# Optimization experiments

Hardware: AMD Instinct MI355X
Metric: run time of the kernel (lower is better)

## Reference

```python
import jax, jax.numpy as jnp
import numpy as np

BN_EPS = 1e-3  # Keras BatchNormalization default epsilon

def _conv2d_same(x, w, b):
    # x: NHWC, w: HWIO (kh,kw,2,1)
    y = jax.lax.conv_general_dilated(x, w, window_strides=(1, 1), padding='SAME',
                                     dimension_numbers=('NHWC', 'HWIO', 'NHWC'))
    return y + b

def _zpool(t):
    # concat([max, avg], axis=-1) over channel axis -> last dim = 2
    return jnp.concatenate([jnp.max(t, axis=-1, keepdims=True),
                            jnp.mean(t, axis=-1, keepdims=True)], axis=-1)

def _att_map(t2, w, b, g, beta, mean, var):
    y = _conv2d_same(t2, w, b)
    y = (y - mean) * jax.lax.rsqrt(var + BN_EPS) * g + beta  # inference BN
    return jax.nn.sigmoid(y)

def setup_inputs() -> dict:
    key = jax.random.key(0)
    ks = jax.random.split(key, 8)
    B, H, W, C, K, RR = 32, 56, 56, 256, 7, 8
    d = {}
    d['x'] = jax.random.normal(ks[0], (B, H, W, C), dtype=jnp.float32)
    for i, kk in zip((1, 2, 3), ks[1:4]):
        d[f'conv{i}_w'] = jax.random.normal(kk, (K, K, 2, 1), dtype=jnp.float32) * 0.1
        d[f'conv{i}_b'] = jnp.zeros((1,), dtype=jnp.float32)
        d[f'bn{i}_g'] = jnp.ones((1,), dtype=jnp.float32)
        d[f'bn{i}_b'] = jnp.zeros((1,), dtype=jnp.float32)
        d[f'bn{i}_m'] = jnp.zeros((1,), dtype=jnp.float32)
        d[f'bn{i}_v'] = jnp.ones((1,), dtype=jnp.float32)
    Ch = C // RR
    d['se_w1'] = jax.random.normal(ks[4], (C, Ch), dtype=jnp.float32) * (2.0 / C) ** 0.5
    d['se_b1'] = jnp.zeros((Ch,), dtype=jnp.float32)
    d['se_w2'] = jax.random.normal(ks[5], (Ch, C), dtype=jnp.float32) * 0.05
    d['se_b2'] = jnp.zeros((C,), dtype=jnp.float32)
    return d

def reference(x, conv1_w, conv1_b, bn1_g, bn1_b, bn1_m, bn1_v,
              conv2_w, conv2_b, bn2_g, bn2_b, bn2_m, bn2_v,
              conv3_w, conv3_b, bn3_g, bn3_b, bn3_m, bn3_v,
              se_w1, se_b1, se_w2, se_b2):
    # Branch 1 (H-axis): permute (B,H,W,C)->(B,H,C,W), pool over W
    th1 = jnp.transpose(x, (0, 1, 3, 2))
    a1 = _att_map(_zpool(th1), conv1_w, conv1_b, bn1_g, bn1_b, bn1_m, bn1_v)
    br1 = jnp.transpose(th1 * a1, (0, 1, 3, 2))
    # Branch 2 (W-axis): permute (B,H,W,C)->(B,C,W,H), pool over H
    th2 = jnp.transpose(x, (0, 3, 2, 1))
    a2 = _att_map(_zpool(th2), conv2_w, conv2_b, bn2_g, bn2_b, bn2_m, bn2_v)
    br2 = jnp.transpose(th2 * a2, (0, 3, 2, 1))
    # Branch 3 (identity): pool over C
    a3 = _att_map(_zpool(x), conv3_w, conv3_b, bn3_g, bn3_b, bn3_m, bn3_v)
    br3 = x * a3
    # TriSE1: Add branches, then SE channel gating
    s = br1 + br2 + br3
    gap = jnp.mean(s, axis=(1, 2), keepdims=True)            # (B,1,1,C)
    h = jax.nn.relu(jnp.einsum('bijc,cd->bijd', gap, se_w1) + se_b1)
    cw = jax.nn.sigmoid(jnp.einsum('bijd,dc->bijc', h, se_w2) + se_b2)
    return s * cw
```

## Files before the change

kernel.cpp:

```cpp
#include <hip/hip_runtime.h>
#include <math.h>

namespace {
constexpr int B = 32, H = 56, W = 56, C = 256;
constexpr int HW  = H * W;
constexpr int WC  = W * C;
constexpr int HC  = H * C;
constexpr int HWC = H * W * C;
constexpr int CH  = 32;
constexpr float BN_EPS = 1e-3f;

__device__ __forceinline__ float sigmoidf_(float v) { return 1.0f / (1.0f + expf(-v)); }
}

__global__ __launch_bounds__(256)
void pool13_kernel(const float* __restrict__ x,
                   float* __restrict__ pmax1, float* __restrict__ pavg1,
                   float* __restrict__ pmax3, float* __restrict__ pavg3) {
    const int b = blockIdx.x / H, h = blockIdx.x % H;
    const int t = threadIdx.x;
    const int lane = t & 63, sub = t >> 6;
    const int c4 = lane * 4;
    const float* xp = x + (size_t)b * HWC + (size_t)h * WC;

    float4 mx = make_float4(-INFINITY, -INFINITY, -INFINITY, -INFINITY);
    float4 sm = make_float4(0.f, 0.f, 0.f, 0.f);
    for (int wq = 0; wq < 14; ++wq) {
        const int w = wq * 4 + sub;
        const float4 v = *(const float4*)(xp + w * C + c4);
        mx.x = fmaxf(mx.x, v.x); mx.y = fmaxf(mx.y, v.y);
        mx.z = fmaxf(mx.z, v.z); mx.w = fmaxf(mx.w, v.w);
        sm.x += v.x; sm.y += v.y; sm.z += v.z; sm.w += v.w;
        float m3 = fmaxf(fmaxf(v.x, v.y), fmaxf(v.z, v.w));
        float s3 = v.x + v.y + v.z + v.w;
        #pragma unroll
        for (int off = 32; off > 0; off >>= 1) {
            m3 = fmaxf(m3, __shfl_down(m3, off));
            s3 += __shfl_down(s3, off);
        }
        if (lane == 0) {
            pmax3[b * HW + h * W + w] = m3;
            pavg3[b * HW + h * W + w] = s3 * (1.0f / C);
        }
    }
    __shared__ float smx[4][256];
    __shared__ float ssm[4][256];
    *(float4*)&smx[sub][c4] = mx;
    *(float4*)&ssm[sub][c4] = sm;
    __syncthreads();
    const float m = fmaxf(fmaxf(smx[0][t], smx[1][t]), fmaxf(smx[2][t], smx[3][t]));
    const float s = ssm[0][t] + ssm[1][t] + ssm[2][t] + ssm[3][t];
    pmax1[b * HC + h * C + t] = m;
    pavg1[b * HC + h * C + t] = s * (1.0f / W);
}

__global__ __launch_bounds__(256)
void pool2_kernel(const float* __restrict__ x,
                  float* __restrict__ pmax2, float* __restrict__ pavg2) {
    const int b = blockIdx.x / W, w = blockIdx.x % W;
    const int t = threadIdx.x;
    const int lane = t & 63, sub = t >> 6;
    const int c4 = lane * 4;
    const float* xp = x + (size_t)b * HWC + (size_t)w * C;

    float4 mx = make_float4(-INFINITY, -INFINITY, -INFINITY, -INFINITY);
    float4 sm = make_float4(0.f, 0.f, 0.f, 0.f);
    for (int hq = 0; hq < 14; ++hq) {
        const int h = hq * 4 + sub;
        const float4 v = *(const float4*)(xp + (size_t)h * WC + c4);
        mx.x = fmaxf(mx.x, v.x); mx.y = fmaxf(mx.y, v.y);
        mx.z = fmaxf(mx.z, v.z); mx.w = fmaxf(mx.w, v.w);
        sm.x += v.x; sm.y += v.y; sm.z += v.z; sm.w += v.w;
    }
    __shared__ float smx[4][256];
    __shared__ float ssm[4][256];
    *(float4*)&smx[sub][c4] = mx;
    *(float4*)&ssm[sub][c4] = sm;
    __syncthreads();
    const float m = fmaxf(fmaxf(smx[0][t], smx[1][t]), fmaxf(smx[2][t], smx[3][t]));
    const float s = ssm[0][t] + ssm[1][t] + ssm[2][t] + ssm[3][t];
    pmax2[b * WC + w * C + t] = m;
    pavg2[b * WC + w * C + t] = s * (1.0f / H);
}

__global__ __launch_bounds__(256)
void conv1_kernel(const float* __restrict__ pmax, const float* __restrict__ pavg,
                  const float* __restrict__ cwt, const float* __restrict__ cb,
                  const float* __restrict__ g, const float* __restrict__ beta,
                  const float* __restrict__ mean, const float* __restrict__ var,
                  float* __restrict__ a1) {
    const int b = blockIdx.x / H, h = blockIdx.x % H;
    const int c = threadIdx.x;
    __shared__ float wg[98];
    if (c < 98) wg[c] = cwt[c];
    __syncthreads();
    const float A  = rsqrtf(var[0] + BN_EPS) * g[0];
    const float Bc = (cb[0] - mean[0]) * A + beta[0];
    float acc = 0.f;
    const float* bm = pmax + b * HC;
    const float* ba = pavg + b * HC;
    #pragma unroll
    for (int ky = 0; ky < 7; ++ky) {
        const int hy = h + ky - 3;
        if (hy < 0 || hy >= H) continue;
        const float* rm = bm + hy * C;
        const float* ra = ba + hy * C;
        #pragma unroll
        for (int kx = 0; kx < 7; ++kx) {
            const int cx = c + kx - 3;
            if (cx < 0 || cx >= C) continue;
            acc += rm[cx] * wg[ky * 14 + kx * 2] + ra[cx] * wg[ky * 14 + kx * 2 + 1];
        }
    }
    a1[b * HC + h * C + c] = sigmoidf_(acc * A + Bc);
}

__global__ __launch_bounds__(256)
void conv2_kernel(const float* __restrict__ pmax, const float* __restrict__ pavg,
                  const float* __restrict__ cwt, const float* __restrict__ cb,
                  const float* __restrict__ g, const float* __restrict__ beta,
                  const float* __restrict__ mean, const float* __restrict__ var,
                  float* __restrict__ a2t) {
    const int b = blockIdx.x / W, w = blockIdx.x % W;
    const int c = threadIdx.x;
    __shared__ float wg[98];
    if (c < 98) wg[c] = cwt[c];
    __syncthreads();
    const float A  = rsqrtf(var[0] + BN_EPS) * g[0];
    const float Bc = (cb[0] - mean[0]) * A + beta[0];
    float acc = 0.f;
    #pragma unroll
    for (int kx = 0; kx < 7; ++kx) {
        const int wx = w + kx - 3;
        if (wx < 0 || wx >= W) continue;
        const float* rm = pmax + b * WC + wx * C;
        const float* ra = pavg + b * WC + wx * C;
        #pragma unroll
        for (int ky = 0; ky < 7; ++ky) {
            const int cy = c + ky - 3;
            if (cy < 0 || cy >= C) continue;
            acc += rm[cy] * wg[ky * 14 + kx * 2] + ra[cy] * wg[ky * 14 + kx * 2 + 1];
        }
    }
    a2t[b * WC + w * C + c] = sigmoidf_(acc * A + Bc);
}

__global__ __launch_bounds__(256)
void conv3_kernel(const float* __restrict__ pmax, const float* __restrict__ pavg,
                  const float* __restrict__ cwt, const float* __restrict__ cb,
                  const float* __restrict__ g, const float* __restrict__ beta,
                  const float* __restrict__ mean, const float* __restrict__ var,
                  float* __restrict__ a3) {
    const int b = blockIdx.x / 13;
    const int idx = (blockIdx.x % 13) * 256 + threadIdx.x;
    __shared__ float wg[98];
    if (threadIdx.x < 98) wg[threadIdx.x] = cwt[threadIdx.x];
    __syncthreads();
    if (idx >= HW) return;
    const int h = idx / W, w = idx % W;
    const float A  = rsqrtf(var[0] + BN_EPS) * g[0];
    const float Bc = (cb[0] - mean[0]) * A + beta[0];
    float acc = 0.f;
    const float* bm = pmax + b * HW;
    const float* ba = pavg + b * HW;
    #pragma unroll
    for (int ky = 0; ky < 7; ++ky) {
        const int hy = h + ky - 3;
        if (hy < 0 || hy >= H) continue;
        #pragma unroll
        for (int kx = 0; kx < 7; ++kx) {
            const int wx = w + kx - 3;
            if (wx < 0 || wx >= W) continue;
            acc += bm[hy * W + wx] * wg[ky * 14 + kx * 2] + ba[hy * W + wx] * wg[ky * 14 + kx * 2 + 1];
        }
    }
    a3[b * HW + idx] = sigmoidf_(acc * A + Bc);
}

__global__ __launch_bounds__(256)
void gap_kernel(const float* __restrict__ x, const float* __restrict__ a1,
                const float* __restrict__ a2t, const float* __restrict__ a3,
                float* __restrict__ gap) {
    const int b = blockIdx.x / H, h = blockIdx.x % H;
    const int t = threadIdx.x;
    const int lane = t & 63, sub = t >> 6;
    const int c4 = lane * 4;
    const float* xp  = x   + (size_t)b * HWC + (size_t)h * WC;
    const float* a2b = a2t + (size_t)b * WC;
    const float4 a1v = *(const float4*)(a1 + b * HC + h * C + c4);
    float4 acc = make_float4(0.f, 0.f, 0.f, 0.f);
    for (int wq = 0; wq < 14; ++wq) {
        const int w = wq * 4 + sub;
        const float4 xv  = *(const float4*)(xp  + w * C + c4);
        const float4 a2v = *(const float4*)(a2b + w * C + c4);
        const float a3v  = a3[b * HW + h * W + w];
        acc.x += xv.x * (a1v.x + a2v.x + a3v);
        acc.y += xv.y * (a1v.y + a2v.y + a3v);
        acc.z += xv.z * (a1v.z + a2v.z + a3v);
        acc.w += xv.w * (a1v.w + a2v.w + a3v);
    }
    __shared__ float sacc[4][256];
    *(float4*)&sacc[sub][c4] = acc;
    __syncthreads();
    const float s = sacc[0][t] + sacc[1][t] + sacc[2][t] + sacc[3][t];
    atomicAdd(&gap[b * C + t], s * (1.0f / (float)HW));
}

__global__ __launch_bounds__(256)
void se_kernel(const float* __restrict__ gap,
               const float* __restrict__ w1, const float* __restrict__ b1,
               const float* __restrict__ w2, const float* __restrict__ b2,
               float* __restrict__ cw) {
    const int b = blockIdx.x;
    const int t = threadIdx.x;
    __shared__ float gs[C];
    __shared__ float hs[CH];
    gs[t] = gap[b * C + t];
    __syncthreads();
    if (t < CH) {
        float a = b1[t];
        for (int c = 0; c < C; ++c) a += gs[c] * w1[c * CH + t];
        hs[t] = fmaxf(a, 0.f);
    }
    __syncthreads();
    float a = b2[t];
    #pragma unroll
    for (int d = 0; d < CH; ++d) a += hs[d] * w2[d * C + t];
    cw[b * C + t] = sigmoidf_(a);
}

__global__ __launch_bounds__(256)
void out_kernel(const float* __restrict__ x, const float* __restrict__ a1,
                const float* __restrict__ a2t, const float* __restrict__ a3,
                const float* __restrict__ cw, float* __restrict__ out) {
    const int r = blockIdx.x * 4 + (threadIdx.x >> 6);
    const int b = r / HW;
    const int hw = r % HW;
    const int h = hw / W, w = hw % W;
    const int c = (threadIdx.x & 63) * 4;
    const float4 xv  = *(const float4*)(x   + (size_t)r * C + c);
    const float4 a1v = *(const float4*)(a1  + b * HC + h * C + c);
    const float4 a2v = *(const float4*)(a2t + b * WC + w * C + c);
    const float  a3v = a3[r];
    const float4 cwv = *(const float4*)(cw  + b * C + c);
    float4 o;
    o.x = xv.x * (a1v.x + a2v.x + a3v) * cwv.x;
    o.y = xv.y * (a1v.y + a2v.y + a3v) * cwv.y;
    o.z = xv.z * (a1v.z + a2v.z + a3v) * cwv.z;
    o.w = xv.w * (a1v.w + a2v.w + a3v) * cwv.w;
    *(float4*)(out + (size_t)r * C + c) = o;
}

extern "C" void kernel_launch(void* const* d_in, const int* in_sizes, int n_in,
                              void* d_out, int out_size, void* d_ws, size_t ws_size,
                              hipStream_t stream) {
    const float* x = (const float*)d_in[0];
    const float* c1w = (const float*)d_in[1];  const float* c1b = (const float*)d_in[2];
    const float* g1  = (const float*)d_in[3];  const float* be1 = (const float*)d_in[4];
    const float* m1  = (const float*)d_in[5];  const float* v1  = (const float*)d_in[6];
    const float* c2w = (const float*)d_in[7];  const float* c2b = (const float*)d_in[8];
    const float* g2  = (const float*)d_in[9];  const float* be2 = (const float*)d_in[10];
    const float* m2  = (const float*)d_in[11]; const float* v2  = (const float*)d_in[12];
    const float* c3w = (const float*)d_in[13]; const float* c3b = (const float*)d_in[14];
    const float* g3  = (const float*)d_in[15]; const float* be3 = (const float*)d_in[16];
    const float* m3  = (const float*)d_in[17]; const float* v3  = (const float*)d_in[18];
    const float* sw1 = (const float*)d_in[19]; const float* sb1 = (const float*)d_in[20];
    const float* sw2 = (const float*)d_in[21]; const float* sb2 = (const float*)d_in[22];

    float* ws = (float*)d_ws;
    float* pmax1 = ws;
    float* pavg1 = pmax1 + (size_t)B * HC;
    float* pmax2 = pavg1 + (size_t)B * HC;
    float* pavg2 = pmax2 + (size_t)B * WC;
    float* pmax3 = pavg2 + (size_t)B * WC;
    float* pavg3 = pmax3 + (size_t)B * HW;
    float* a1    = pavg3 + (size_t)B * HW;
    float* a2t   = a1    + (size_t)B * HC;
    float* a3    = a2t   + (size_t)B * WC;
    float* gap   = a3    + (size_t)B * HW;
    float* cwv   = gap   + (size_t)B * C;

    hipMemsetAsync(gap, 0, (size_t)B * C * sizeof(float), stream);

    pool13_kernel<<<B * H, 256, 0, stream>>>(x, pmax1, pavg1, pmax3, pavg3);
    pool2_kernel <<<B * W, 256, 0, stream>>>(x, pmax2, pavg2);
    conv1_kernel <<<B * H, 256, 0, stream>>>(pmax1, pavg1, c1w, c1b, g1, be1, m1, v1, a1);
    conv2_kernel <<<B * W, 256, 0, stream>>>(pmax2, pavg2, c2w, c2b, g2, be2, m2, v2, a2t);
    conv3_kernel <<<B * 13, 256, 0, stream>>>(pmax3, pavg3, c3w, c3b, g3, be3, m3, v3, a3);
    gap_kernel   <<<B * H, 256, 0, stream>>>(x, a1, a2t, a3, gap);
    se_kernel    <<<B, 256, 0, stream>>>(gap, sw1, sb1, sw2, sb2, cwv);
    out_kernel   <<<B * HW / 4, 256, 0, stream>>>(x, a1, a2t, a3, cwv, (float*)d_out);
}
```

Before: 325.9 us.

## Fuse all stages into one persistent cooperative kernel with grid syncs

Replaces the eight separate launches and the memset with a single cooperative persistent kernel. Its blocks loop over task lists for pooling, the three convolutions, the GAP partial sums, the SE MLP and the output, with grid.sync between phases. The GAP atomics become per-task partial sums that are reduced deterministically in the SE phase. This is meant to remove launch overhead and tail gaps between small kernels. In exchange it adds grid-wide barriers, limits the grid size to occupancy, and leaves most blocks idle during the SE phase, which only B blocks run.

```diff
diff --git a/kernel.cpp b/kernel.cpp
--- a/kernel.cpp
+++ b/kernel.cpp
@@ -1,5 +1,8 @@
 #include <hip/hip_runtime.h>
+#include <hip/hip_cooperative_groups.h>
 #include <math.h>
+
+namespace cg = cooperative_groups;
 
 namespace {
 constexpr int B = 32, H = 56, W = 56, C = 256;
@@ -10,251 +13,258 @@
 constexpr int CH  = 32;
 constexpr float BN_EPS = 1e-3f;
 
+constexpr int NPOOL_TASKS = 2 * B * H;
+constexpr int NCONV_TASKS = B * H + B * W + (B * HW) / 256;
+constexpr int NHALF_TASKS = B * H * 2;
+
 __device__ __forceinline__ float sigmoidf_(float v) { return 1.0f / (1.0f + expf(-v)); }
 }
 
-__global__ __launch_bounds__(256)
-void pool13_kernel(const float* __restrict__ x,
-                   float* __restrict__ pmax1, float* __restrict__ pavg1,
-                   float* __restrict__ pmax3, float* __restrict__ pavg3) {
-    const int b = blockIdx.x / H, h = blockIdx.x % H;
-    const int t = threadIdx.x;
-    const int lane = t & 63, sub = t >> 6;
-    const int c4 = lane * 4;
-    const float* xp = x + (size_t)b * HWC + (size_t)h * WC;
-
-    float4 mx = make_float4(-INFINITY, -INFINITY, -INFINITY, -INFINITY);
-    float4 sm = make_float4(0.f, 0.f, 0.f, 0.f);
-    for (int wq = 0; wq < 14; ++wq) {
-        const int w = wq * 4 + sub;
-        const float4 v = *(const float4*)(xp + w * C + c4);
-        mx.x = fmaxf(mx.x, v.x); mx.y = fmaxf(mx.y, v.y);
-        mx.z = fmaxf(mx.z, v.z); mx.w = fmaxf(mx.w, v.w);
-        sm.x += v.x; sm.y += v.y; sm.z += v.z; sm.w += v.w;
-        float m3 = fmaxf(fmaxf(v.x, v.y), fmaxf(v.z, v.w));
-        float s3 = v.x + v.y + v.z + v.w;
-        #pragma unroll
-        for (int off = 32; off > 0; off >>= 1) {
-            m3 = fmaxf(m3, __shfl_down(m3, off));
-            s3 += __shfl_down(s3, off);
-        }
-        if (lane == 0) {
-            pmax3[b * HW + h * W + w] = m3;
-            pavg3[b * HW + h * W + w] = s3 * (1.0f / C);
-        }
-    }
+__global__ __launch_bounds__(256, 4)
+void fused_trise_kernel(const float* __restrict__ x,
+                        const float* __restrict__ c1w, const float* __restrict__ c1b,
+                        const float* __restrict__ g1,  const float* __restrict__ be1,
+                        const float* __restrict__ m1,  const float* __restrict__ v1,
+                        const float* __restrict__ c2w, const float* __restrict__ c2b,
+                        const float* __restrict__ g2,  const float* __restrict__ be2,
+                        const float* __restrict__ m2,  const float* __restrict__ v2,
+                        const float* __restrict__ c3w, const float* __restrict__ c3b,
+                        const float* __restrict__ g3,  const float* __restrict__ be3,
+                        const float* __restrict__ m3,  const float* __restrict__ v3,
+                        const float* __restrict__ sw1, const float* __restrict__ sb1,
+                        const float* __restrict__ sw2, const float* __restrict__ sb2,
+                        float* __restrict__ ws, float* __restrict__ out) {
+    float* pmax1 = ws;
+    float* pavg1 = pmax1 + (size_t)B * HC;
+    float* pmax2 = pavg1 + (size_t)B * HC;
+    float* pavg2 = pmax2 + (size_t)B * WC;
+    float* pmax3 = pavg2 + (size_t)B * WC;
+    float* pavg3 = pmax3 + (size_t)B * HW;
+    float* a1    = pavg3 + (size_t)B * HW;
+    float* a2t   = a1    + (size_t)B * HC;
+    float* a3    = a2t   + (size_t)B * WC;
+    float* gpart = a3    + (size_t)B * HW;
+    float* cw    = gpart + (size_t)NHALF_TASKS * C;
+
     __shared__ float smx[4][256];
     __shared__ float ssm[4][256];
-    *(float4*)&smx[sub][c4] = mx;
-    *(float4*)&ssm[sub][c4] = sm;
-    __syncthreads();
-    const float m = fmaxf(fmaxf(smx[0][t], smx[1][t]), fmaxf(smx[2][t], smx[3][t]));
-    const float s = ssm[0][t] + ssm[1][t] + ssm[2][t] + ssm[3][t];
-    pmax1[b * HC + h * C + t] = m;
-    pavg1[b * HC + h * C + t] = s * (1.0f / W);
-}
-
-__global__ __launch_bounds__(256)
-void pool2_kernel(const float* __restrict__ x,
-                  float* __restrict__ pmax2, float* __restrict__ pavg2) {
-    const int b = blockIdx.x / W, w = blockIdx.x % W;
-    const int t = threadIdx.x;
+    __shared__ float wc0[98], wc1[98], wc2[98];
+    __shared__ float sbnA[3], sbnB[3];
+    __shared__ float gs[C];
+    __shared__ float hsh[CH];
+
+    const int nb   = gridDim.x;
+    const int t    = threadIdx.x;
     const int lane = t & 63, sub = t >> 6;
-    const int c4 = lane * 4;
-    const float* xp = x + (size_t)b * HWC + (size_t)w * C;
-
-    float4 mx = make_float4(-INFINITY, -INFINITY, -INFINITY, -INFINITY);
-    float4 sm = make_float4(0.f, 0.f, 0.f, 0.f);
-    for (int hq = 0; hq < 14; ++hq) {
-        const int h = hq * 4 + sub;
-        const float4 v = *(const float4*)(xp + (size_t)h * WC + c4);
-        mx.x = fmaxf(mx.x, v.x); mx.y = fmaxf(mx.y, v.y);
-        mx.z = fmaxf(mx.z, v.z); mx.w = fmaxf(mx.w, v.w);
-        sm.x += v.x; sm.y += v.y; sm.z += v.z; sm.w += v.w;
-    }
-    __shared__ float smx[4][256];
-    __shared__ float ssm[4][256];
-    *(float4*)&smx[sub][c4] = mx;
-    *(float4*)&ssm[sub][c4] = sm;
-    __syncthreads();
-    const float m = fmaxf(fmaxf(smx[0][t], smx[1][t]), fmaxf(smx[2][t], smx[3][t]));
-    const float s = ssm[0][t] + ssm[1][t] + ssm[2][t] + ssm[3][t];
-    pmax2[b * WC + w * C + t] = m;
-    pavg2[b * WC + w * C + t] = s * (1.0f / H);
-}
-
-__global__ __launch_bounds__(256)
-void conv1_kernel(const float* __restrict__ pmax, const float* __restrict__ pavg,
-                  const float* __restrict__ cwt, const float* __restrict__ cb,
-                  const float* __restrict__ g, const float* __restrict__ beta,
-                  const float* __restrict__ mean, const float* __restrict__ var,
-                  float* __restrict__ a1) {
-    const int b = blockIdx.x / H, h = blockIdx.x % H;
-    const int c = threadIdx.x;
-    __shared__ float wg[98];
-    if (c < 98) wg[c] = cwt[c];
-    __syncthreads();
-    const float A  = rsqrtf(var[0] + BN_EPS) * g[0];
-    const float Bc = (cb[0] - mean[0]) * A + beta[0];
-    float acc = 0.f;
-    const float* bm = pmax + b * HC;
-    const float* ba = pavg + b * HC;
-    #pragma unroll
-    for (int ky = 0; ky < 7; ++ky) {
-        const int hy = h + ky - 3;
-        if (hy < 0 || hy >= H) continue;
-        const float* rm = bm + hy * C;
-        const float* ra = ba + hy * C;
+    const int c4   = lane * 4;
+
+    if (t < 98) { wc0[t] = c1w[t]; wc1[t] = c2w[t]; wc2[t] = c3w[t]; }
+    if (t == 0) { float A = rsqrtf(v1[0] + BN_EPS) * g1[0]; sbnA[0] = A; sbnB[0] = (c1b[0] - m1[0]) * A + be1[0]; }
+    if (t == 1) { float A = rsqrtf(v2[0] + BN_EPS) * g2[0]; sbnA[1] = A; sbnB[1] = (c2b[0] - m2[0]) * A + be2[0]; }
+    if (t == 2) { float A = rsqrtf(v3[0] + BN_EPS) * g3[0]; sbnA[2] = A; sbnB[2] = (c3b[0] - m3[0]) * A + be3[0]; }
+
+    cg::grid_group grid = cg::this_grid();
+
+    for (int tt = blockIdx.x; tt < NPOOL_TASKS; tt += nb) {
+        if (tt < B * H) {
+            const int b = tt / H, h = tt % H;
+            const float* xp = x + (size_t)b * HWC + (size_t)h * WC;
+            float4 mx = make_float4(-INFINITY, -INFINITY, -INFINITY, -INFINITY);
+            float4 sm = make_float4(0.f, 0.f, 0.f, 0.f);
+            for (int wq = 0; wq < 14; ++wq) {
+                const int w = wq * 4 + sub;
+                const float4 v = *(const float4*)(xp + w * C + c4);
+                mx.x = fmaxf(mx.x, v.x); mx.y = fmaxf(mx.y, v.y);
+                mx.z = fmaxf(mx.z, v.z); mx.w = fmaxf(mx.w, v.w);
+                sm.x += v.x; sm.y += v.y; sm.z += v.z; sm.w += v.w;
+                float m3v = fmaxf(fmaxf(v.x, v.y), fmaxf(v.z, v.w));
+                float s3v = v.x + v.y + v.z + v.w;
+                #pragma unroll
+                for (int off = 32; off > 0; off >>= 1) {
+                    m3v = fmaxf(m3v, __shfl_down(m3v, off));
+                    s3v += __shfl_down(s3v, off);
+                }
+                if (lane == 0) {
+                    pmax3[b * HW + h * W + w] = m3v;
+                    pavg3[b * HW + h * W + w] = s3v * (1.0f / C);
+                }
+            }
+            __syncthreads();
+            *(float4*)&smx[sub][c4] = mx;
+            *(float4*)&ssm[sub][c4] = sm;
+            __syncthreads();
+            const float m = fmaxf(fmaxf(smx[0][t], smx[1][t]), fmaxf(smx[2][t], smx[3][t]));
+            const float s = ssm[0][t] + ssm[1][t] + ssm[2][t] + ssm[3][t];
+            pmax1[b * HC + h * C + t] = m;
+            pavg1[b * HC + h * C + t] = s * (1.0f / W);
+        } else {
+            const int tt2 = tt - B * H;
+            const int b = tt2 / W, w = tt2 % W;
+            const float* xp = x + (size_t)b * HWC + (size_t)w * C;
+            float4 mx = make_float4(-INFINITY, -INFINITY, -INFINITY, -INFINITY);
+            float4 sm = make_float4(0.f, 0.f, 0.f, 0.f);
+            for (int hq = 0; hq < 14; ++hq) {
+                const int h = hq * 4 + sub;
+                const float4 v = *(const float4*)(xp + (size_t)h * WC + c4);
+                mx.x = fmaxf(mx.x, v.x); mx.y = fmaxf(mx.y, v.y);
+                mx.z = fmaxf(mx.z, v.z); mx.w = fmaxf(mx.w, v.w);
+                sm.x += v.x; sm.y += v.y; sm.z += v.z; sm.w += v.w;
+            }
+            __syncthreads();
+            *(float4*)&smx[sub][c4] = mx;
+            *(float4*)&ssm[sub][c4] = sm;
+            __syncthreads();
+            const float m = fmaxf(fmaxf(smx[0][t], smx[1][t]), fmaxf(smx[2][t], smx[3][t]));
+            const float s = ssm[0][t] + ssm[1][t] + ssm[2][t] + ssm[3][t];
+            pmax2[b * WC + w * C + t] = m;
+            pavg2[b * WC + w * C + t] = s * (1.0f / H);
+        }
+    }
+    __threadfence();
+    grid.sync();
+
+    for (int tt = blockIdx.x; tt < NCONV_TASKS; tt += nb) {
+        if (tt < B * H) {
+            const int b = tt / H, h = tt % H;
+            const int c = t;
+            const float A = sbnA[0], Bc = sbnB[0];
+            float acc = 0.f;
+            const float* bm = pmax1 + b * HC;
+            const float* ba = pavg1 + b * HC;
+            #pragma unroll
+            for (int ky = 0; ky < 7; ++ky) {
+                const int hy = h + ky - 3;
+                if (hy < 0 || hy >= H) continue;
+                const float* rm = bm + hy * C;
+                const float* ra = ba + hy * C;
+                #pragma unroll
+                for (int kx = 0; kx < 7; ++kx) {
+                    const int cx = c + kx - 3;
+                    if (cx < 0 || cx >= C) continue;
+                    acc += rm[cx] * wc0[ky * 14 + kx * 2] + ra[cx] * wc0[ky * 14 + kx * 2 + 1];
+                }
+            }
+            a1[b * HC + h * C + c] = sigmoidf_(acc * A + Bc);
+        } else if (tt < 2 * B * H) {
+            const int tt2 = tt - B * H;
+            const int b = tt2 / W, w = tt2 % W;
+            const int c = t;
+            const float A = sbnA[1], Bc = sbnB[1];
+            float acc = 0.f;
+            #pragma unroll
+            for (int kx = 0; kx < 7; ++kx) {
+                const int wx = w + kx - 3;
+                if (wx < 0 || wx >= W) continue;
+                const float* rm = pmax2 + b * WC + wx * C;
+                const float* ra = pavg2 + b * WC + wx * C;
+                #pragma unroll
+                for (int ky = 0; ky < 7; ++ky) {
+                    const int cy = c + ky - 3;
+                    if (cy < 0 || cy >= C) continue;
+                    acc += rm[cy] * wc1[ky * 14 + kx * 2] + ra[cy] * wc1[ky * 14 + kx * 2 + 1];
+                }
+            }
+            a2t[b * WC + w * C + c] = sigmoidf_(acc * A + Bc);
+        } else {
+            const int gid = (tt - 2 * B * H) * 256 + t;
+            const int b = gid / HW;
+            const int hw = gid % HW;
+            const int h = hw / W, w = hw % W;
+            const float A = sbnA[2], Bc = sbnB[2];
+            float acc = 0.f;
+            const float* bm = pmax3 + b * HW;
+            const float* ba = pavg3 + b * HW;
+            #pragma unroll
+            for (int ky = 0; ky < 7; ++ky) {
+                const int hy = h + ky - 3;
+                if (hy < 0 || hy >= H) continue;
+                #pragma unroll
+                for (int kx = 0; kx < 7; ++kx) {
+                    const int wx = w + kx - 3;
+                    if (wx < 0 || wx >= W) continue;
+                    acc += bm[hy * W + wx] * wc2[ky * 14 + kx * 2] + ba[hy * W + wx] * wc2[ky * 14 + kx * 2 + 1];
+                }
+            }
+            a3[b * HW + hw] = sigmoidf_(acc * A + Bc);
+        }
+    }
+    __threadfence();
+    grid.sync();
+
+    for (int tt = blockIdx.x; tt < NHALF_TASKS; tt += nb) {
+        const int b = tt / (2 * H);
+        const int rem = tt % (2 * H);
+        const int h = rem >> 1, half = rem & 1;
+        const float* xp  = x   + (size_t)b * HWC + (size_t)h * WC;
+        const float* a2b = a2t + (size_t)b * WC;
+        const float4 a1v = *(const float4*)(a1 + b * HC + h * C + c4);
+        float4 acc = make_float4(0.f, 0.f, 0.f, 0.f);
+        for (int wq = 0; wq < 7; ++wq) {
+            const int w = half * 28 + wq * 4 + sub;
+            const float4 xv  = *(const float4*)(xp  + w * C + c4);
+            const float4 a2v = *(const float4*)(a2b + w * C + c4);
+            const float a3v  = a3[b * HW + h * W + w];
+            acc.x += xv.x * (a1v.x + a2v.x + a3v);
+            acc.y += xv.y * (a1v.y + a2v.y + a3v);
+            acc.z += xv.z * (a1v.z + a2v.z + a3v);
+            acc.w += xv.w * (a1v.w + a2v.w + a3v);
+        }
+        __syncthreads();
+        *(float4*)&smx[sub][c4] = acc;
+        __syncthreads();
+        gpart[(size_t)tt * C + t] = smx[0][t] + smx[1][t] + smx[2][t] + smx[3][t];
+    }
+    __threadfence();
+    grid.sync();
+
+    if (blockIdx.x < B) {
+        const int b = blockIdx.x;
+        float s = 0.f;
+        for (int r = 0; r < 2 * H; ++r) s += gpart[(size_t)(b * 2 * H + r) * C + t];
+        gs[t] = s * (1.0f / (float)HW);
+        __syncthreads();
+        if (t < CH) {
+            float a = sb1[t];
+            for (int c = 0; c < C; ++c) a += gs[c] * sw1[c * CH + t];
+            hsh[t] = fmaxf(a, 0.f);
+        }
+        __syncthreads();
+        float a = sb2[t];
         #pragma unroll
-        for (int kx = 0; kx < 7; ++kx) {
-            const int cx = c + kx - 3;
-            if (cx < 0 || cx >= C) continue;
-            acc += rm[cx] * wg[ky * 14 + kx * 2] + ra[cx] * wg[ky * 14 + kx * 2 + 1];
-        }
-    }
-    a1[b * HC + h * C + c] = sigmoidf_(acc * A + Bc);
-}
-
-__global__ __launch_bounds__(256)
-void conv2_kernel(const float* __restrict__ pmax, const float* __restrict__ pavg,
-                  const float* __restrict__ cwt, const float* __restrict__ cb,
-                  const float* __restrict__ g, const float* __restrict__ beta,
-                  const float* __restrict__ mean, const float* __restrict__ var,
-                  float* __restrict__ a2t) {
-    const int b = blockIdx.x / W, w = blockIdx.x % W;
-    const int c = threadIdx.x;
-    __shared__ float wg[98];
-    if (c < 98) wg[c] = cwt[c];
-    __syncthreads();
-    const float A  = rsqrtf(var[0] + BN_EPS) * g[0];
-    const float Bc = (cb[0] - mean[0]) * A + beta[0];
-    float acc = 0.f;
-    #pragma unroll
-    for (int kx = 0; kx < 7; ++kx) {
-        const int wx = w + kx - 3;
-        if (wx < 0 || wx >= W) continue;
-        const float* rm = pmax + b * WC + wx * C;
-        const float* ra = pavg + b * WC + wx * C;
-        #pragma unroll
-        for (int ky = 0; ky < 7; ++ky) {
-            const int cy = c + ky - 3;
-            if (cy < 0 || cy >= C) continue;
-            acc += rm[cy] * wg[ky * 14 + kx * 2] + ra[cy] * wg[ky * 14 + kx * 2 + 1];
-        }
-    }
-    a2t[b * WC + w * C + c] = sigmoidf_(acc * A + Bc);
-}
-
-__global__ __launch_bounds__(256)
-void conv3_kernel(const float* __restrict__ pmax, const float* __restrict__ pavg,
-                  const float* __restrict__ cwt, const float* __restrict__ cb,
-                  const float* __restrict__ g, const float* __restrict__ beta,
-                  const float* __restrict__ mean, const float* __restrict__ var,
-                  float* __restrict__ a3) {
-    const int b = blockIdx.x / 13;
-    const int idx = (blockIdx.x % 13) * 256 + threadIdx.x;
-    __shared__ float wg[98];
-    if (threadIdx.x < 98) wg[threadIdx.x] = cwt[threadIdx.x];
-    __syncthreads();
-    if (idx >= HW) return;
-    const int h = idx / W, w = idx % W;
-    const float A  = rsqrtf(var[0] + BN_EPS) * g[0];
-    const float Bc = (cb[0] - mean[0]) * A + beta[0];
-    float acc = 0.f;
-    const float* bm = pmax + b * HW;
-    const float* ba = pavg + b * HW;
-    #pragma unroll
-    for (int ky = 0; ky < 7; ++ky) {
-        const int hy = h + ky - 3;
-        if (hy < 0 || hy >= H) continue;
-        #pragma unroll
-        for (int kx = 0; kx < 7; ++kx) {
-            const int wx = w + kx - 3;
-            if (wx < 0 || wx >= W) continue;
-            acc += bm[hy * W + wx] * wg[ky * 14 + kx * 2] + ba[hy * W + wx] * wg[ky * 14 + kx * 2 + 1];
-        }
-    }
-    a3[b * HW + idx] = sigmoidf_(acc * A + Bc);
-}
-
-__global__ __launch_bounds__(256)
-void gap_kernel(const float* __restrict__ x, const float* __restrict__ a1,
-                const float* __restrict__ a2t, const float* __restrict__ a3,
-                float* __restrict__ gap) {
-    const int b = blockIdx.x / H, h = blockIdx.x % H;
-    const int t = threadIdx.x;
-    const int lane = t & 63, sub = t >> 6;
-    const int c4 = lane * 4;
-    const float* xp  = x   + (size_t)b * HWC + (size_t)h * WC;
-    const float* a2b = a2t + (size_t)b * WC;
-    const float4 a1v = *(const float4*)(a1 + b * HC + h * C + c4);
-    float4 acc = make_float4(0.f, 0.f, 0.f, 0.f);
-    for (int wq = 0; wq < 14; ++wq) {
-        const int w = wq * 4 + sub;
-        const float4 xv  = *(const float4*)(xp  + w * C + c4);
-        const float4 a2v = *(const float4*)(a2b + w * C + c4);
-        const float a3v  = a3[b * HW + h * W + w];
-        acc.x += xv.x * (a1v.x + a2v.x + a3v);
-        acc.y += xv.y * (a1v.y + a2v.y + a3v);
-        acc.z += xv.z * (a1v.z + a2v.z + a3v);
-        acc.w += xv.w * (a1v.w + a2v.w + a3v);
-    }
-    __shared__ float sacc[4][256];
-    *(float4*)&sacc[sub][c4] = acc;
-    __syncthreads();
-    const float s = sacc[0][t] + sacc[1][t] + sacc[2][t] + sacc[3][t];
-    atomicAdd(&gap[b * C + t], s * (1.0f / (float)HW));
-}
-
-__global__ __launch_bounds__(256)
-void se_kernel(const float* __restrict__ gap,
-               const float* __restrict__ w1, const float* __restrict__ b1,
-               const float* __restrict__ w2, const float* __restrict__ b2,
-               float* __restrict__ cw) {
-    const int b = blockIdx.x;
-    const int t = threadIdx.x;
-    __shared__ float gs[C];
-    __shared__ float hs[CH];
-    gs[t] = gap[b * C + t];
-    __syncthreads();
-    if (t < CH) {
-        float a = b1[t];
-        for (int c = 0; c < C; ++c) a += gs[c] * w1[c * CH + t];
-        hs[t] = fmaxf(a, 0.f);
-    }
-    __syncthreads();
-    float a = b2[t];
-    #pragma unroll
-    for (int d = 0; d < CH; ++d) a += hs[d] * w2[d * C + t];
-    cw[b * C + t] = sigmoidf_(a);
-}
-
-__global__ __launch_bounds__(256)
-void out_kernel(const float* __restrict__ x, const float* __restrict__ a1,
-                const float* __restrict__ a2t, const float* __restrict__ a3,
-                const float* __restrict__ cw, float* __restrict__ out) {
-    const int r = blockIdx.x * 4 + (threadIdx.x >> 6);
-    const int b = r / HW;
-    const int hw = r % HW;
-    const int h = hw / W, w = hw % W;
-    const int c = (threadIdx.x & 63) * 4;
-    const float4 xv  = *(const float4*)(x   + (size_t)r * C + c);
-    const float4 a1v = *(const float4*)(a1  + b * HC + h * C + c);
-    const float4 a2v = *(const float4*)(a2t + b * WC + w * C + c);
-    const float  a3v = a3[r];
-    const float4 cwv = *(const float4*)(cw  + b * C + c);
-    float4 o;
-    o.x = xv.x * (a1v.x + a2v.x + a3v) * cwv.x;
-    o.y = xv.y * (a1v.y + a2v.y + a3v) * cwv.y;
-    o.z = xv.z * (a1v.z + a2v.z + a3v) * cwv.z;
-    o.w = xv.w * (a1v.w + a2v.w + a3v) * cwv.w;
-    *(float4*)(out + (size_t)r * C + c) = o;
+        for (int d = 0; d < CH; ++d) a += hsh[d] * sw2[d * C + t];
+        cw[b * C + t] = sigmoidf_(a);
+    }
+    __threadfence();
+    grid.sync();
+
+    for (int tt = blockIdx.x; tt < NHALF_TASKS; tt += nb) {
+        const int b = tt / (2 * H);
+        const int rem = tt % (2 * H);
+        const int h = rem >> 1, half = rem & 1;
+        const float* xp  = x   + (size_t)b * HWC + (size_t)h * WC;
+        const float* a2b = a2t + (size_t)b * WC;
+        float*       op  = out + (size_t)b * HWC + (size_t)h * WC;
+        const float4 a1v = *(const float4*)(a1 + b * HC + h * C + c4);
+        const float4 cwv = *(const float4*)(cw + b * C + c4);
+        for (int wq = 0; wq < 7; ++wq) {
+            const int w = half * 28 + wq * 4 + sub;
+            const float4 xv  = *(const float4*)(xp  + w * C + c4);
+            const float4 a2v = *(const float4*)(a2b + w * C + c4);
+            const float a3v  = a3[b * HW + h * W + w];
+            float4 o;
+            o.x = xv.x * (a1v.x + a2v.x + a3v) * cwv.x;
+            o.y = xv.y * (a1v.y + a2v.y + a3v) * cwv.y;
+            o.z = xv.z * (a1v.z + a2v.z + a3v) * cwv.z;
+            o.w = xv.w * (a1v.w + a2v.w + a3v) * cwv.w;
+            *(float4*)(op + w * C + c4) = o;
+        }
+    }
 }
 
 extern "C" void kernel_launch(void* const* d_in, const int* in_sizes, int n_in,
                               void* d_out, int out_size, void* d_ws, size_t ws_size,
                               hipStream_t stream) {
-    const float* x = (const float*)d_in[0];
+    const float* x   = (const float*)d_in[0];
     const float* c1w = (const float*)d_in[1];  const float* c1b = (const float*)d_in[2];
     const float* g1  = (const float*)d_in[3];  const float* be1 = (const float*)d_in[4];
     const float* m1  = (const float*)d_in[5];  const float* v1  = (const float*)d_in[6];
@@ -266,28 +276,23 @@
     const float* m3  = (const float*)d_in[17]; const float* v3  = (const float*)d_in[18];
     const float* sw1 = (const float*)d_in[19]; const float* sb1 = (const float*)d_in[20];
     const float* sw2 = (const float*)d_in[21]; const float* sb2 = (const float*)d_in[22];
-
-    float* ws = (float*)d_ws;
-    float* pmax1 = ws;
-    float* pavg1 = pmax1 + (size_t)B * HC;
-    float* pmax2 = pavg1 + (size_t)B * HC;
-    float* pavg2 = pmax2 + (size_t)B * WC;
-    float* pmax3 = pavg2 + (size_t)B * WC;
-    float* pavg3 = pmax3 + (size_t)B * HW;
-    float* a1    = pavg3 + (size_t)B * HW;
-    float* a2t   = a1    + (size_t)B * HC;
-    float* a3    = a2t   + (size_t)B * WC;
-    float* gap   = a3    + (size_t)B * HW;
-    float* cwv   = gap   + (size_t)B * C;
-
-    hipMemsetAsync(gap, 0, (size_t)B * C * sizeof(float), stream);
-
-    pool13_kernel<<<B * H, 256, 0, stream>>>(x, pmax1, pavg1, pmax3, pavg3);
-    pool2_kernel <<<B * W, 256, 0, stream>>>(x, pmax2, pavg2);
-    conv1_kernel <<<B * H, 256, 0, stream>>>(pmax1, pavg1, c1w, c1b, g1, be1, m1, v1, a1);
-    conv2_kernel <<<B * W, 256, 0, stream>>>(pmax2, pavg2, c2w, c2b, g2, be2, m2, v2, a2t);
-    conv3_kernel <<<B * 13, 256, 0, stream>>>(pmax3, pavg3, c3w, c3b, g3, be3, m3, v3, a3);
-    gap_kernel   <<<B * H, 256, 0, stream>>>(x, a1, a2t, a3, gap);
-    se_kernel    <<<B, 256, 0, stream>>>(gap, sw1, sb1, sw2, sb2, cwv);
-    out_kernel   <<<B * HW / 4, 256, 0, stream>>>(x, a1, a2t, a3, cwv, (float*)d_out);
+    float* ws  = (float*)d_ws;
+    float* out = (float*)d_out;
+
+    int nbpc = 0;
+    hipOccupancyMaxActiveBlocksPerMultiprocessor(&nbpc, fused_trise_kernel, 256, 0);
+    if (nbpc < 1) nbpc = 1;
+    int grid = nbpc * 256;
+    if (grid > NPOOL_TASKS) grid = NPOOL_TASKS;
+
+    void* args[] = {
+        (void*)&x,
+        (void*)&c1w, (void*)&c1b, (void*)&g1, (void*)&be1, (void*)&m1, (void*)&v1,
+        (void*)&c2w, (void*)&c2b, (void*)&g2, (void*)&be2, (void*)&m2, (void*)&v2,
+        (void*)&c3w, (void*)&c3b, (void*)&g3, (void*)&be3, (void*)&m3, (void*)&v3,
+        (void*)&sw1, (void*)&sb1, (void*)&sw2, (void*)&sb2,
+        (void*)&ws, (void*)&out,
+    };
+    hipLaunchCooperativeKernel((const void*)fused_trise_kernel, dim3(grid), dim3(256),
+                               args, 0, stream);
 }
```

Result: slower. 879.1 us (+169.8%).

## Merge pool and conv launches, replace atomic GAP with partials, row-wise output

Applied to the files above, without the earlier changes.

Combines the two pooling kernels into one launch and the three conv kernels into one branch-dispatched launch, cutting the launch count and letting small grids overlap. The global-average-pool atomics and their memset are replaced by per-row partial sums that the SE kernel reduces. The output kernel now processes one row per block, reusing the a1 and cw loads across 14 width steps. The trade-offs are a larger partial-sum workspace and divergent block roles inside the merged kernels.

```diff
diff --git a/kernel.cpp b/kernel.cpp
--- a/kernel.cpp
+++ b/kernel.cpp
@@ -14,173 +14,162 @@
 }
 
 __global__ __launch_bounds__(256)
-void pool13_kernel(const float* __restrict__ x,
-                   float* __restrict__ pmax1, float* __restrict__ pavg1,
-                   float* __restrict__ pmax3, float* __restrict__ pavg3) {
-    const int b = blockIdx.x / H, h = blockIdx.x % H;
+void pool_all_kernel(const float* __restrict__ x,
+                     float* __restrict__ pmax1, float* __restrict__ pavg1,
+                     float* __restrict__ pmax2, float* __restrict__ pavg2,
+                     float* __restrict__ pmax3, float* __restrict__ pavg3) {
     const int t = threadIdx.x;
     const int lane = t & 63, sub = t >> 6;
     const int c4 = lane * 4;
-    const float* xp = x + (size_t)b * HWC + (size_t)h * WC;
-
-    float4 mx = make_float4(-INFINITY, -INFINITY, -INFINITY, -INFINITY);
-    float4 sm = make_float4(0.f, 0.f, 0.f, 0.f);
-    for (int wq = 0; wq < 14; ++wq) {
-        const int w = wq * 4 + sub;
-        const float4 v = *(const float4*)(xp + w * C + c4);
-        mx.x = fmaxf(mx.x, v.x); mx.y = fmaxf(mx.y, v.y);
-        mx.z = fmaxf(mx.z, v.z); mx.w = fmaxf(mx.w, v.w);
-        sm.x += v.x; sm.y += v.y; sm.z += v.z; sm.w += v.w;
-        float m3 = fmaxf(fmaxf(v.x, v.y), fmaxf(v.z, v.w));
-        float s3 = v.x + v.y + v.z + v.w;
-        #pragma unroll
-        for (int off = 32; off > 0; off >>= 1) {
-            m3 = fmaxf(m3, __shfl_down(m3, off));
-            s3 += __shfl_down(s3, off);
-        }
-        if (lane == 0) {
-            pmax3[b * HW + h * W + w] = m3;
-            pavg3[b * HW + h * W + w] = s3 * (1.0f / C);
-        }
-    }
     __shared__ float smx[4][256];
     __shared__ float ssm[4][256];
-    *(float4*)&smx[sub][c4] = mx;
-    *(float4*)&ssm[sub][c4] = sm;
-    __syncthreads();
-    const float m = fmaxf(fmaxf(smx[0][t], smx[1][t]), fmaxf(smx[2][t], smx[3][t]));
-    const float s = ssm[0][t] + ssm[1][t] + ssm[2][t] + ssm[3][t];
-    pmax1[b * HC + h * C + t] = m;
-    pavg1[b * HC + h * C + t] = s * (1.0f / W);
-}
-
-__global__ __launch_bounds__(256)
-void pool2_kernel(const float* __restrict__ x,
-                  float* __restrict__ pmax2, float* __restrict__ pavg2) {
-    const int b = blockIdx.x / W, w = blockIdx.x % W;
-    const int t = threadIdx.x;
-    const int lane = t & 63, sub = t >> 6;
-    const int c4 = lane * 4;
-    const float* xp = x + (size_t)b * HWC + (size_t)w * C;
-
-    float4 mx = make_float4(-INFINITY, -INFINITY, -INFINITY, -INFINITY);
-    float4 sm = make_float4(0.f, 0.f, 0.f, 0.f);
-    for (int hq = 0; hq < 14; ++hq) {
-        const int h = hq * 4 + sub;
-        const float4 v = *(const float4*)(xp + (size_t)h * WC + c4);
-        mx.x = fmaxf(mx.x, v.x); mx.y = fmaxf(mx.y, v.y);
-        mx.z = fmaxf(mx.z, v.z); mx.w = fmaxf(mx.w, v.w);
-        sm.x += v.x; sm.y += v.y; sm.z += v.z; sm.w += v.w;
-    }
-    __shared__ float smx[4][256];
-    __shared__ float ssm[4][256];
-    *(float4*)&smx[sub][c4] = mx;
-    *(float4*)&ssm[sub][c4] = sm;
-    __syncthreads();
-    const float m = fmaxf(fmaxf(smx[0][t], smx[1][t]), fmaxf(smx[2][t], smx[3][t]));
-    const float s = ssm[0][t] + ssm[1][t] + ssm[2][t] + ssm[3][t];
-    pmax2[b * WC + w * C + t] = m;
-    pavg2[b * WC + w * C + t] = s * (1.0f / H);
-}
-
-__global__ __launch_bounds__(256)
-void conv1_kernel(const float* __restrict__ pmax, const float* __restrict__ pavg,
-                  const float* __restrict__ cwt, const float* __restrict__ cb,
-                  const float* __restrict__ g, const float* __restrict__ beta,
-                  const float* __restrict__ mean, const float* __restrict__ var,
-                  float* __restrict__ a1) {
-    const int b = blockIdx.x / H, h = blockIdx.x % H;
-    const int c = threadIdx.x;
+
+    if (blockIdx.x < B * H) {
+        const int b = blockIdx.x / H, h = blockIdx.x % H;
+        const float* xp = x + (size_t)b * HWC + (size_t)h * WC;
+        float4 mx = make_float4(-INFINITY, -INFINITY, -INFINITY, -INFINITY);
+        float4 sm = make_float4(0.f, 0.f, 0.f, 0.f);
+        for (int wq = 0; wq < 14; ++wq) {
+            const int w = wq * 4 + sub;
+            const float4 v = *(const float4*)(xp + w * C + c4);
+            mx.x = fmaxf(mx.x, v.x); mx.y = fmaxf(mx.y, v.y);
+            mx.z = fmaxf(mx.z, v.z); mx.w = fmaxf(mx.w, v.w);
+            sm.x += v.x; sm.y += v.y; sm.z += v.z; sm.w += v.w;
+            float m3 = fmaxf(fmaxf(v.x, v.y), fmaxf(v.z, v.w));
+            float s3 = v.x + v.y + v.z + v.w;
+            #pragma unroll
+            for (int off = 32; off > 0; off >>= 1) {
+                m3 = fmaxf(m3, __shfl_down(m3, off));
+                s3 += __shfl_down(s3, off);
+            }
+            if (lane == 0) {
+                pmax3[b * HW + h * W + w] = m3;
+                pavg3[b * HW + h * W + w] = s3 * (1.0f / C);
+            }
+        }
+        *(float4*)&smx[sub][c4] = mx;
+        *(float4*)&ssm[sub][c4] = sm;
+        __syncthreads();
+        const float m = fmaxf(fmaxf(smx[0][t], smx[1][t]), fmaxf(smx[2][t], smx[3][t]));
+        const float s = ssm[0][t] + ssm[1][t] + ssm[2][t] + ssm[3][t];
+        pmax1[b * HC + h * C + t] = m;
+        pavg1[b * HC + h * C + t] = s * (1.0f / W);
+    } else {
+        const int tt = blockIdx.x - B * H;
+        const int b = tt / W, w = tt % W;
+        const float* xp = x + (size_t)b * HWC + (size_t)w * C;
+        float4 mx = make_float4(-INFINITY, -INFINITY, -INFINITY, -INFINITY);
+        float4 sm = make_float4(0.f, 0.f, 0.f, 0.f);
+        for (int hq = 0; hq < 14; ++hq) {
+            const int h = hq * 4 + sub;
+            const float4 v = *(const float4*)(xp + (size_t)h * WC + c4);
+            mx.x = fmaxf(mx.x, v.x); mx.y = fmaxf(mx.y, v.y);
+            mx.z = fmaxf(mx.z, v.z); mx.w = fmaxf(mx.w, v.w);
+            sm.x += v.x; sm.y += v.y; sm.z += v.z; sm.w += v.w;
+        }
+        *(float4*)&smx[sub][c4] = mx;
+        *(float4*)&ssm[sub][c4] = sm;
+        __syncthreads();
+        const float m = fmaxf(fmaxf(smx[0][t], smx[1][t]), fmaxf(smx[2][t], smx[3][t]));
+        const float s = ssm[0][t] + ssm[1][t] + ssm[2][t] + ssm[3][t];
+        pmax2[b * WC + w * C + t] = m;
+        pavg2[b * WC + w * C + t] = s * (1.0f / H);
+    }
+}
+
+__global__ __launch_bounds__(256)
+void conv_all_kernel(const float* __restrict__ pmax1, const float* __restrict__ pavg1,
+                     const float* __restrict__ pmax2, const float* __restrict__ pavg2,
+                     const float* __restrict__ pmax3, const float* __restrict__ pavg3,
+                     const float* __restrict__ c1w, const float* __restrict__ c1b,
+                     const float* __restrict__ g1,  const float* __restrict__ be1,
+                     const float* __restrict__ m1,  const float* __restrict__ v1,
+                     const float* __restrict__ c2w, const float* __restrict__ c2b,
+                     const float* __restrict__ g2,  const float* __restrict__ be2,
+                     const float* __restrict__ m2,  const float* __restrict__ v2,
+                     const float* __restrict__ c3w, const float* __restrict__ c3b,
+                     const float* __restrict__ g3,  const float* __restrict__ be3,
+                     const float* __restrict__ m3,  const float* __restrict__ v3,
+                     float* __restrict__ a1, float* __restrict__ a2t, float* __restrict__ a3) {
+    const int t = threadIdx.x;
     __shared__ float wg[98];
-    if (c < 98) wg[c] = cwt[c];
-    __syncthreads();
-    const float A  = rsqrtf(var[0] + BN_EPS) * g[0];
-    const float Bc = (cb[0] - mean[0]) * A + beta[0];
-    float acc = 0.f;
-    const float* bm = pmax + b * HC;
-    const float* ba = pavg + b * HC;
-    #pragma unroll
-    for (int ky = 0; ky < 7; ++ky) {
-        const int hy = h + ky - 3;
-        if (hy < 0 || hy >= H) continue;
-        const float* rm = bm + hy * C;
-        const float* ra = ba + hy * C;
-        #pragma unroll
-        for (int kx = 0; kx < 7; ++kx) {
-            const int cx = c + kx - 3;
-            if (cx < 0 || cx >= C) continue;
-            acc += rm[cx] * wg[ky * 14 + kx * 2] + ra[cx] * wg[ky * 14 + kx * 2 + 1];
-        }
-    }
-    a1[b * HC + h * C + c] = sigmoidf_(acc * A + Bc);
-}
-
-__global__ __launch_bounds__(256)
-void conv2_kernel(const float* __restrict__ pmax, const float* __restrict__ pavg,
-                  const float* __restrict__ cwt, const float* __restrict__ cb,
-                  const float* __restrict__ g, const float* __restrict__ beta,
-                  const float* __restrict__ mean, const float* __restrict__ var,
-                  float* __restrict__ a2t) {
-    const int b = blockIdx.x / W, w = blockIdx.x % W;
-    const int c = threadIdx.x;
-    __shared__ float wg[98];
-    if (c < 98) wg[c] = cwt[c];
-    __syncthreads();
-    const float A  = rsqrtf(var[0] + BN_EPS) * g[0];
-    const float Bc = (cb[0] - mean[0]) * A + beta[0];
-    float acc = 0.f;
-    #pragma unroll
-    for (int kx = 0; kx < 7; ++kx) {
-        const int wx = w + kx - 3;
-        if (wx < 0 || wx >= W) continue;
-        const float* rm = pmax + b * WC + wx * C;
-        const float* ra = pavg + b * WC + wx * C;
+
+    if (blockIdx.x < B * H) {
+        if (t < 98) wg[t] = c1w[t];
+        __syncthreads();
+        const int b = blockIdx.x / H, h = blockIdx.x % H;
+        const float A  = rsqrtf(v1[0] + BN_EPS) * g1[0];
+        const float Bc = (c1b[0] - m1[0]) * A + be1[0];
+        float acc = 0.f;
+        const float* bm = pmax1 + b * HC;
+        const float* ba = pavg1 + b * HC;
         #pragma unroll
         for (int ky = 0; ky < 7; ++ky) {
-            const int cy = c + ky - 3;
-            if (cy < 0 || cy >= C) continue;
-            acc += rm[cy] * wg[ky * 14 + kx * 2] + ra[cy] * wg[ky * 14 + kx * 2 + 1];
-        }
-    }
-    a2t[b * WC + w * C + c] = sigmoidf_(acc * A + Bc);
-}
-
-__global__ __launch_bounds__(256)
-void conv3_kernel(const float* __restrict__ pmax, const float* __restrict__ pavg,
-                  const float* __restrict__ cwt, const float* __restrict__ cb,
-                  const float* __restrict__ g, const float* __restrict__ beta,
-                  const float* __restrict__ mean, const float* __restrict__ var,
-                  float* __restrict__ a3) {
-    const int b = blockIdx.x / 13;
-    const int idx = (blockIdx.x % 13) * 256 + threadIdx.x;
-    __shared__ float wg[98];
-    if (threadIdx.x < 98) wg[threadIdx.x] = cwt[threadIdx.x];
-    __syncthreads();
-    if (idx >= HW) return;
-    const int h = idx / W, w = idx % W;
-    const float A  = rsqrtf(var[0] + BN_EPS) * g[0];
-    const float Bc = (cb[0] - mean[0]) * A + beta[0];
-    float acc = 0.f;
-    const float* bm = pmax + b * HW;
-    const float* ba = pavg + b * HW;
-    #pragma unroll
-    for (int ky = 0; ky < 7; ++ky) {
-        const int hy = h + ky - 3;
-        if (hy < 0 || hy >= H) continue;
+            const int hy = h + ky - 3;
+            if (hy < 0 || hy >= H) continue;
+            const float* rm = bm + hy * C;
+            const float* ra = ba + hy * C;
+            #pragma unroll
+            for (int kx = 0; kx < 7; ++kx) {
+                const int cx = t + kx - 3;
+                if (cx < 0 || cx >= C) continue;
+                acc += rm[cx] * wg[ky * 14 + kx * 2] + ra[cx] * wg[ky * 14 + kx * 2 + 1];
+            }
+        }
+        a1[b * HC + h * C + t] = sigmoidf_(acc * A + Bc);
+    } else if (blockIdx.x < 2 * B * H) {
+        if (t < 98) wg[t] = c2w[t];
+        __syncthreads();
+        const int tt = blockIdx.x - B * H;
+        const int b = tt / W, w = tt % W;
+        const float A  = rsqrtf(v2[0] + BN_EPS) * g2[0];
+        const float Bc = (c2b[0] - m2[0]) * A + be2[0];
+        float acc = 0.f;
         #pragma unroll
         for (int kx = 0; kx < 7; ++kx) {
             const int wx = w + kx - 3;
             if (wx < 0 || wx >= W) continue;
-            acc += bm[hy * W + wx] * wg[ky * 14 + kx * 2] + ba[hy * W + wx] * wg[ky * 14 + kx * 2 + 1];
-        }
-    }
-    a3[b * HW + idx] = sigmoidf_(acc * A + Bc);
-}
-
-__global__ __launch_bounds__(256)
-void gap_kernel(const float* __restrict__ x, const float* __restrict__ a1,
-                const float* __restrict__ a2t, const float* __restrict__ a3,
-                float* __restrict__ gap) {
+            const float* rm = pmax2 + b * WC + wx * C;
+            const float* ra = pavg2 + b * WC + wx * C;
+            #pragma unroll
+            for (int ky = 0; ky < 7; ++ky) {
+                const int cy = t + ky - 3;
+                if (cy < 0 || cy >= C) continue;
+                acc += rm[cy] * wg[ky * 14 + kx * 2] + ra[cy] * wg[ky * 14 + kx * 2 + 1];
+            }
+        }
+        a2t[b * WC + w * C + t] = sigmoidf_(acc * A + Bc);
+    } else {
+        if (t < 98) wg[t] = c3w[t];
+        __syncthreads();
+        const int gid = (blockIdx.x - 2 * B * H) * 256 + t;
+        const int b = gid / HW;
+        const int hw = gid % HW;
+        const int h = hw / W, w = hw % W;
+        const float A  = rsqrtf(v3[0] + BN_EPS) * g3[0];
+        const float Bc = (c3b[0] - m3[0]) * A + be3[0];
+        float acc = 0.f;
+        const float* bm = pmax3 + b * HW;
+        const float* ba = pavg3 + b * HW;
+        #pragma unroll
+        for (int ky = 0; ky < 7; ++ky) {
+            const int hy = h + ky - 3;
+            if (hy < 0 || hy >= H) continue;
+            #pragma unroll
+            for (int kx = 0; kx < 7; ++kx) {
+                const int wx = w + kx - 3;
+                if (wx < 0 || wx >= W) continue;
+                acc += bm[hy * W + wx] * wg[ky * 14 + kx * 2] + ba[hy * W + wx] * wg[ky * 14 + kx * 2 + 1];
+            }
+        }
+        a3[b * HW + hw] = sigmoidf_(acc * A + Bc);
+    }
+}
+
+__global__ __launch_bounds__(256)
+void gap_row_kernel(const float* __restrict__ x, const float* __restrict__ a1,
+                    const float* __restrict__ a2t, const float* __restrict__ a3,
+                    float* __restrict__ gpart) {
     const int b = blockIdx.x / H, h = blockIdx.x % H;
     const int t = threadIdx.x;
     const int lane = t & 63, sub = t >> 6;
@@ -202,12 +191,11 @@
     __shared__ float sacc[4][256];
     *(float4*)&sacc[sub][c4] = acc;
     __syncthreads();
-    const float s = sacc[0][t] + sacc[1][t] + sacc[2][t] + sacc[3][t];
-    atomicAdd(&gap[b * C + t], s * (1.0f / (float)HW));
-}
-
-__global__ __launch_bounds__(256)
-void se_kernel(const float* __restrict__ gap,
+    gpart[(size_t)blockIdx.x * C + t] = sacc[0][t] + sacc[1][t] + sacc[2][t] + sacc[3][t];
+}
+
+__global__ __launch_bounds__(256)
+void se_kernel(const float* __restrict__ gpart,
                const float* __restrict__ w1, const float* __restrict__ b1,
                const float* __restrict__ w2, const float* __restrict__ b2,
                float* __restrict__ cw) {
@@ -215,7 +203,9 @@
     const int t = threadIdx.x;
     __shared__ float gs[C];
     __shared__ float hs[CH];
-    gs[t] = gap[b * C + t];
+    float s = 0.f;
+    for (int r = 0; r < H; ++r) s += gpart[(size_t)(b * H + r) * C + t];
+    gs[t] = s * (1.0f / (float)HW);
     __syncthreads();
     if (t < CH) {
         float a = b1[t];
@@ -230,31 +220,36 @@
 }
 
 __global__ __launch_bounds__(256)
-void out_kernel(const float* __restrict__ x, const float* __restrict__ a1,
-                const float* __restrict__ a2t, const float* __restrict__ a3,
-                const float* __restrict__ cw, float* __restrict__ out) {
-    const int r = blockIdx.x * 4 + (threadIdx.x >> 6);
-    const int b = r / HW;
-    const int hw = r % HW;
-    const int h = hw / W, w = hw % W;
-    const int c = (threadIdx.x & 63) * 4;
-    const float4 xv  = *(const float4*)(x   + (size_t)r * C + c);
-    const float4 a1v = *(const float4*)(a1  + b * HC + h * C + c);
-    const float4 a2v = *(const float4*)(a2t + b * WC + w * C + c);
-    const float  a3v = a3[r];
-    const float4 cwv = *(const float4*)(cw  + b * C + c);
-    float4 o;
-    o.x = xv.x * (a1v.x + a2v.x + a3v) * cwv.x;
-    o.y = xv.y * (a1v.y + a2v.y + a3v) * cwv.y;
-    o.z = xv.z * (a1v.z + a2v.z + a3v) * cwv.z;
-    o.w = xv.w * (a1v.w + a2v.w + a3v) * cwv.w;
-    *(float4*)(out + (size_t)r * C + c) = o;
+void out_row_kernel(const float* __restrict__ x, const float* __restrict__ a1,
+                    const float* __restrict__ a2t, const float* __restrict__ a3,
+                    const float* __restrict__ cw, float* __restrict__ out) {
+    const int b = blockIdx.x / H, h = blockIdx.x % H;
+    const int t = threadIdx.x;
+    const int lane = t & 63, sub = t >> 6;
+    const int c4 = lane * 4;
+    const float* xp  = x   + (size_t)b * HWC + (size_t)h * WC;
+    const float* a2b = a2t + (size_t)b * WC;
+    float*       op  = out + (size_t)b * HWC + (size_t)h * WC;
+    const float4 a1v = *(const float4*)(a1 + b * HC + h * C + c4);
+    const float4 cwv = *(const float4*)(cw + b * C + c4);
+    for (int wq = 0; wq < 14; ++wq) {
+        const int w = wq * 4 + sub;
+        const float4 xv  = *(const float4*)(xp  + w * C + c4);
+        const float4 a2v = *(const float4*)(a2b + w * C + c4);
+        const float a3v  = a3[b * HW + h * W + w];
+        float4 o;
+        o.x = xv.x * (a1v.x + a2v.x + a3v) * cwv.x;
+        o.y = xv.y * (a1v.y + a2v.y + a3v) * cwv.y;
+        o.z = xv.z * (a1v.z + a2v.z + a3v) * cwv.z;
+        o.w = xv.w * (a1v.w + a2v.w + a3v) * cwv.w;
+        *(float4*)(op + w * C + c4) = o;
+    }
 }
 
 extern "C" void kernel_launch(void* const* d_in, const int* in_sizes, int n_in,
                               void* d_out, int out_size, void* d_ws, size_t ws_size,
                               hipStream_t stream) {
-    const float* x = (const float*)d_in[0];
+    const float* x   = (const float*)d_in[0];
     const float* c1w = (const float*)d_in[1];  const float* c1b = (const float*)d_in[2];
     const float* g1  = (const float*)d_in[3];  const float* be1 = (const float*)d_in[4];
     const float* m1  = (const float*)d_in[5];  const float* v1  = (const float*)d_in[6];
@@ -277,17 +272,17 @@
     float* a1    = pavg3 + (size_t)B * HW;
     float* a2t   = a1    + (size_t)B * HC;
     float* a3    = a2t   + (size_t)B * WC;
-    float* gap   = a3    + (size_t)B * HW;
-    float* cwv   = gap   + (size_t)B * C;
-
-    hipMemsetAsync(gap, 0, (size_t)B * C * sizeof(float), stream);
-
-    pool13_kernel<<<B * H, 256, 0, stream>>>(x, pmax1, pavg1, pmax3, pavg3);
-    pool2_kernel <<<B * W, 256, 0, stream>>>(x, pmax2, pavg2);
-    conv1_kernel <<<B * H, 256, 0, stream>>>(pmax1, pavg1, c1w, c1b, g1, be1, m1, v1, a1);
-    conv2_kernel <<<B * W, 256, 0, stream>>>(pmax2, pavg2, c2w, c2b, g2, be2, m2, v2, a2t);
-    conv3_kernel <<<B * 13, 256, 0, stream>>>(pmax3, pavg3, c3w, c3b, g3, be3, m3, v3, a3);
-    gap_kernel   <<<B * H, 256, 0, stream>>>(x, a1, a2t, a3, gap);
-    se_kernel    <<<B, 256, 0, stream>>>(gap, sw1, sb1, sw2, sb2, cwv);
-    out_kernel   <<<B * HW / 4, 256, 0, stream>>>(x, a1, a2t, a3, cwv, (float*)d_out);
-}
+    float* gpart = a3    + (size_t)B * HW;
+    float* cwv   = gpart + (size_t)B * H * C;
+
+    pool_all_kernel<<<B * H + B * W, 256, 0, stream>>>(x, pmax1, pavg1, pmax2, pavg2, pmax3, pavg3);
+    conv_all_kernel<<<2 * B * H + (B * HW) / 256, 256, 0, stream>>>(
+        pmax1, pavg1, pmax2, pavg2, pmax3, pavg3,
+        c1w, c1b, g1, be1, m1, v1,
+        c2w, c2b, g2, be2, m2, v2,
+        c3w, c3b, g3, be3, m3, v3,
+        a1, a2t, a3);
+    gap_row_kernel<<<B * H, 256, 0, stream>>>(x, a1, a2t, a3, gpart);
+    se_kernel<<<B, 256, 0, stream>>>(gpart, sw1, sb1, sw2, sb2, cwv);
+    out_row_kernel<<<B * H, 256, 0, stream>>>(x, a1, a2t, a3, cwv, (float*)d_out);
+}
```

Result: faster. 311.9 us (-4.3%).
